# Kernel optimization log

Measured on AMD Instinct MI355X. Metric: run time of the kernel, lower is better.

Reference implementation:

```python
import jax, jax.numpy as jnp
import numpy as np

# ---- dims ----
V, VR, E, H, NF = 100000, 5000, 300, 256, 150
H2 = 2 * H  # 512


def _lstm_dir(x, Wih, Whh, b, h0, c0):
    # x: (T, B, E); returns hs (T, B, H), final (h, c)
    def step(carry, xt):
        h, c = carry
        z = xt @ Wih.T + h @ Whh.T + b
        i, f, g, o = jnp.split(z, 4, axis=-1)  # torch gate order i,f,g,o
        c = jax.nn.sigmoid(f) * c + jax.nn.sigmoid(i) * jnp.tanh(g)
        h = jax.nn.sigmoid(o) * jnp.tanh(c)
        return (h, c), h
    (hT, cT), hs = jax.lax.scan(step, (h0, c0), x)
    return hs, hT, cT


def bilstm(x, Wih_f, Whh_f, b_f, Wih_b, Whh_b, b_b, state=None):
    # x: (T, B, E) -> out (T, B, 2H), state tuple
    B = x.shape[1]
    if state is None:
        z = jnp.zeros((B, H), x.dtype)
        state = (z, z, z, z)
    h0f, c0f, h0b, c0b = state
    hs_f, hTf, cTf = _lstm_dir(x, Wih_f, Whh_f, b_f, h0f, c0f)
    hs_b, hTb, cTb = _lstm_dir(x[::-1], Wih_b, Whh_b, b_b, h0b, c0b)
    out = jnp.concatenate([hs_f, hs_b[::-1]], axis=-1)
    return out, (hTf, cTf, hTb, cTb)


def abwim_atten(question_out, word_rel, rela_rel, word_emb, rela_emb,
                Wih_f, Whh_f, b_f, Wih_b, Whh_b, b_b, W):
    # question_out: (B, 2H, Sq); word_rel (B,Sw), rela_rel (B,Sr) int
    rela = rela_emb[rela_rel.T]   # (Sr, B, E)
    word = word_emb[word_rel.T]   # (Sw, B, E)
    word_out, state = bilstm(word, Wih_f, Whh_f, b_f, Wih_b, Whh_b, b_b)
    rela_out, _ = bilstm(rela, Wih_f, Whh_f, b_f, Wih_b, Whh_b, b_b, state)
    relation = jnp.concatenate([rela_out, word_out], axis=0).transpose(1, 0, 2)  # (B, R, 2H)
    energy = jnp.einsum('brh,hk,bks->brs', relation, W, question_out)  # (B, R, Sq)
    B, R, Sq = energy.shape
    scale = 1.0 / np.sqrt(R).astype(np.float32)
    alpha = jax.nn.softmax(energy.reshape(B, R * Sq) * scale, axis=-1).reshape(B, R, Sq)
    # sum_r alpha[b,r,s] * relation[b,r,h] -> (B, 2H, Sq)
    return jnp.einsum('brs,brh->bhs', alpha, relation)


def setup_inputs():
    key = jax.random.key(0)
    ks = jax.random.split(key, 24)
    B, Sq, Sw, Sr = 64, 40, 12, 4
    s_emb, s_lstm, s_w = 0.05, 0.05, 0.04
    inp = {
        'question': jax.random.randint(ks[0], (B, Sq), 0, V),
        'word_relation': jax.random.randint(ks[1], (B, Sw), 0, V),
        'rela_relation': jax.random.randint(ks[2], (B, Sr), 0, VR),
        'word_previous': jax.random.randint(ks[3], (B, Sw), 0, V),
        'rela_previous': jax.random.randint(ks[4], (B, Sr), 0, VR),
        'word_emb': jax.random.normal(ks[5], (V, E), jnp.float32) * s_emb,
        'rela_emb': jax.random.normal(ks[6], (VR, E), jnp.float32) * s_emb,
        'Wih_f': jax.random.normal(ks[7], (4 * H, E), jnp.float32) * s_lstm,
        'Whh_f': jax.random.normal(ks[8], (4 * H, H), jnp.float32) * s_lstm,
        'b_f': jnp.zeros((4 * H,), jnp.float32),
        'Wih_b': jax.random.normal(ks[9], (4 * H, E), jnp.float32) * s_lstm,
        'Whh_b': jax.random.normal(ks[10], (4 * H, H), jnp.float32) * s_lstm,
        'b_b': jnp.zeros((4 * H,), jnp.float32),
        'W': jax.random.normal(ks[11], (H2, H2), jnp.float32) * s_w,
        'cnn1_w': jax.random.normal(ks[12], (NF, 2 * H2, 1), jnp.float32) * s_w,
        'cnn1_b': jnp.zeros((NF,), jnp.float32),
        'cnn2_w': jax.random.normal(ks[13], (NF, 2 * H2, 3), jnp.float32) * s_w,
        'cnn2_b': jnp.zeros((NF,), jnp.float32),
        'cnn3_w': jax.random.normal(ks[14], (NF, 2 * H2, 5), jnp.float32) * s_w,
        'cnn3_b': jnp.zeros((NF,), jnp.float32),
        'lin_w': jax.random.normal(ks[15], (1, NF), jnp.float32) * s_w,
        'lin2_w': jax.random.normal(ks[16], (H2, H2), jnp.float32) * s_w,
        'lin2_b': jnp.zeros((H2,), jnp.float32),
    }
    return inp


def _conv1d(x, w, b):
    # x: (B, C, L), w: (O, C, K)
    y = jax.lax.conv_general_dilated(x, w, (1,), 'VALID',
                                     dimension_numbers=('NCH', 'OIH', 'NCH'))
    return y + b[None, :, None]


def reference(question, word_relation, rela_relation, word_previous, rela_previous,
              word_emb, rela_emb, Wih_f, Whh_f, b_f, Wih_b, Whh_b, b_b, W,
              cnn1_w, cnn1_b, cnn2_w, cnn2_b, cnn3_w, cnn3_b, lin_w, lin2_w, lin2_b):
    lstm_p = (Wih_f, Whh_f, b_f, Wih_b, Whh_b, b_b)
    # question encoder (dropout is identity at eval)
    q = word_emb[question.T]                      # (Sq, B, E)
    q_out, _ = bilstm(q, *lstm_p)                 # (Sq, B, 2H)
    question_out = q_out.transpose(1, 2, 0)       # (B, 2H, Sq)
    # reduce one previous hop
    atten_prev = abwim_atten(question_out, word_previous, rela_previous,
                             word_emb, rela_emb, *lstm_p, W)
    qo = question_out - atten_prev
    qo = qo.transpose(0, 2, 1) @ lin2_w.T + lin2_b   # (B, Sq, 2H)
    question_out = qo.transpose(0, 2, 1)             # (B, 2H, Sq)
    # current relation attention
    atten_relation = abwim_atten(question_out, word_relation, rela_relation,
                                 word_emb, rela_emb, *lstm_p, W)
    M = jnp.concatenate([question_out, atten_relation], axis=1)  # (B, 4H, Sq)
    h1 = jnp.max(jax.nn.relu(_conv1d(M, cnn1_w, cnn1_b)), axis=2)  # (B, NF)
    h2 = jnp.max(jax.nn.relu(_conv1d(M, cnn2_w, cnn2_b)), axis=2)
    h3 = jnp.max(jax.nn.relu(_conv1d(M, cnn3_w, cnn3_b)), axis=2)
    h = jnp.maximum(jnp.maximum(h1, h2), h3)
    score = (h @ lin_w.T).squeeze(-1)  # (B,)
    return score
```

## Files before the change

### kernel.cpp

```cpp
#include <hip/hip_runtime.h>
#include <math.h>

#define NEG_INF (-3.402823466e+38f)

typedef __attribute__((ext_vector_type(8))) short short8;
typedef __attribute__((ext_vector_type(8))) unsigned short ushort8;
typedef __attribute__((ext_vector_type(4))) float f32x4;

constexpr int NTOK = 4608;
constexpr int BH = 64 * 256;

constexpr size_t OFF_WQ    = 0;
constexpr size_t OFF_B2    = OFF_WQ    + 524288;
constexpr size_t OFF_XB3T  = OFF_B2    + 2048;
constexpr size_t OFF_WB3T  = OFF_XB3T  + 983040;
constexpr size_t OFF_L2B3T = OFF_WB3T  + 393216;
constexpr size_t OFF_C1B3T = OFF_L2B3T + 393216;
constexpr size_t OFF_C2B3T = OFF_C1B3T + 294912;
constexpr size_t OFF_C3B3T = OFF_C2B3T + 884736;
constexpr size_t OFF_XHI   = OFF_C3B3T + 1474560;
constexpr size_t OFF_XLO   = OFF_XHI   + 737280;
constexpr size_t OFF_XP    = OFF_XLO   + 737280;
constexpr size_t OFF_HSQ   = OFF_XP    + 9437184;
constexpr size_t OFF_HSWP  = OFF_HSQ   + 1310720;
constexpr size_t OFF_HSRP  = OFF_HSWP  + 393216;
constexpr size_t OFF_HSWR  = OFF_HSRP  + 131072;
constexpr size_t OFF_HSRR  = OFF_HSWR  + 393216;
constexpr size_t OFF_CS    = OFF_HSRR  + 131072;
constexpr size_t OFF_RELP  = OFF_CS    + 163840;
constexpr size_t OFF_RELC  = OFF_RELP  + 524288;
constexpr size_t OFF_RELW  = OFF_RELC  + 524288;
constexpr size_t OFF_EN    = OFF_RELW  + 524288;

__device__ inline unsigned short f2bf(float f) {
  unsigned int u = __float_as_uint(f);
  u += 0x7FFFu + ((u >> 16) & 1u);
  return (unsigned short)(u >> 16);
}
__device__ inline float bf2f(unsigned short h) {
  return __uint_as_float(((unsigned int)h) << 16);
}
__device__ inline short8 mk8(unsigned long long a, unsigned long long b) {
  union { unsigned long long q[2]; short8 s; } u;
  u.q[0] = a; u.q[1] = b; return u.s;
}
#define ALD(p) __hip_atomic_load((p), __ATOMIC_RELAXED, __HIP_MEMORY_SCOPE_AGENT)

__global__ __launch_bounds__(256) void k_prep(
    const float* __restrict__ Whh_f, const float* __restrict__ Whh_b,
    const float* __restrict__ b_f,   const float* __restrict__ b_b,
    const float* __restrict__ Wih_f, const float* __restrict__ Wih_b,
    const float* __restrict__ Wat,   const float* __restrict__ l2w,
    const float* __restrict__ c1w, const float* __restrict__ c2w, const float* __restrict__ c3w,
    unsigned short* __restrict__ WHB, float* __restrict__ B2,
    unsigned short* __restrict__ XB3T, unsigned short* __restrict__ WB3T,
    unsigned short* __restrict__ L2B3T,
    unsigned short* __restrict__ C1B3T, unsigned short* __restrict__ C2B3T,
    unsigned short* __restrict__ C3B3T, int* __restrict__ bar) {
  if (blockIdx.x == 0 && threadIdx.x < 8)
    __hip_atomic_store(bar + threadIdx.x, 0, __ATOMIC_RELAXED, __HIP_MEMORY_SCOPE_AGENT);
  int idx = blockIdx.x * 256 + threadIdx.x;
  if (idx < 1048576) {
    int e = idx & 511;
    int k = e & 255, isLo = e >> 8;
    int row = (idx >> 9) & 63;
    int tile = (idx >> 15) & 15;
    int d = idx >> 19;
    int g = row >> 4, uu = row & 15;
    int u = tile * 16 + uu;
    const float* Wh = d ? Whh_b : Whh_f;
    float w = Wh[(size_t)(g * 256 + u) * 256 + k];
    unsigned short hi = f2bf(w);
    WHB[idx] = isLo ? f2bf(w - bf2f(hi)) : hi;
    return;
  }
  idx -= 1048576;
  if (idx < 2048) { B2[idx] = (idx < 1024) ? b_f[idx] : b_b[idx-1024]; return; }
  idx -= 2048;
  unsigned short* dst; int n, k, K;
  float w;
  if (idx < 655360) {
    n = idx / 320; k = idx % 320; K = 320; dst = XB3T;
    w = (k < 300) ? ((n < 1024) ? Wih_f[(size_t)n*300 + k] : Wih_b[(size_t)(n-1024)*300 + k]) : 0.f;
  } else if ((idx -= 655360) < 262144) {
    n = idx >> 9; k = idx & 511; K = 512; dst = WB3T;
    w = Wat[(size_t)k*512 + n];
  } else if ((idx -= 262144) < 262144) {
    n = idx >> 9; k = idx & 511; K = 512; dst = L2B3T;
    w = l2w[(size_t)n*512 + k];
  } else if ((idx -= 262144) < 196608) {
    n = idx >> 10; k = idx & 1023; K = 1024; dst = C1B3T;
    w = (n < 150) ? c1w[(size_t)n*1024 + k] : 0.f;
  } else if ((idx -= 196608) < 589824) {
    n = idx / 3072; k = idx % 3072; K = 3072; dst = C2B3T;
    int kw = k >> 10, c = k & 1023;
    w = (n < 150) ? c2w[((size_t)n*1024 + c)*3 + kw] : 0.f;
  } else if ((idx -= 589824) < 983040) {
    n = idx / 5120; k = idx % 5120; K = 5120; dst = C3B3T;
    int kw = k >> 10, c = k & 1023;
    w = (n < 150) ? c3w[((size_t)n*1024 + c)*5 + kw] : 0.f;
  } else return;
  unsigned short hi = f2bf(w);
  unsigned short lo = f2bf(w - bf2f(hi));
  size_t base = (size_t)n * (3*K);
  dst[base + k] = hi;
  dst[base + K + k] = lo;
  dst[base + 2*K + k] = hi;
}

__global__ __launch_bounds__(320) void k_gather(
    const int* __restrict__ q,  const int* __restrict__ wr, const int* __restrict__ rr,
    const int* __restrict__ wp, const int* __restrict__ rp,
    const float* __restrict__ we, const float* __restrict__ re,
    unsigned short* __restrict__ Xhi, unsigned short* __restrict__ Xlo) {
  int m = blockIdx.x, k = threadIdx.x;
  const float* emb; int row;
  if (m < 2560)      { int t=m>>6,    b=m&63; row = q [b*40+t]; emb = we; }
  else if (m < 3328) { int mm=m-2560; int t=mm>>6,b=mm&63; row = wp[b*12+t]; emb = we; }
  else if (m < 3584) { int mm=m-3328; int t=mm>>6,b=mm&63; row = rp[b*4 +t]; emb = re; }
  else if (m < 4352) { int mm=m-3584; int t=mm>>6,b=mm&63; row = wr[b*12+t]; emb = we; }
  else               { int mm=m-4352; int t=mm>>6,b=mm&63; row = rr[b*4 +t]; emb = re; }
  float v = (k < 300) ? emb[(size_t)row*300 + k] : 0.f;
  unsigned short hi = f2bf(v);
  Xhi[(size_t)m*320 + k] = hi;
  Xlo[(size_t)m*320 + k] = f2bf(v - bf2f(hi));
}

template<bool BIAS>
__global__ __launch_bounds__(256) void k_mgemm(
    const unsigned short* __restrict__ Ahi, const unsigned short* __restrict__ Alo, int lda,
    const unsigned short* __restrict__ Bt, const float* __restrict__ bias,
    float* __restrict__ C, int N, int K) {
  __shared__ unsigned short As[64 * 40];
  __shared__ unsigned short Bs[64 * 40];
  int tid = threadIdx.x;
  int wave = tid >> 6, lane = tid & 63;
  int quad = lane >> 4, l16 = lane & 15;
  int m0 = blockIdx.x << 6, n0 = blockIdx.y << 6;
  int K3 = 3 * K;
  int sr = tid >> 2;
  int sc = (tid & 3) << 3;
  f32x4 acc[4] = {};
  for (int k0 = 0; k0 < K3; k0 += 32) {
    int c = (k0 >= K) + (k0 >= 2*K);
    const unsigned short* Asrc = (c == 2) ? Alo : Ahi;
    int kk = k0 - c * K;
    ushort8 av = *(const ushort8*)(Asrc + (size_t)(m0 + sr) * lda + kk + sc);
    ushort8 bv = *(const ushort8*)(Bt + (size_t)(n0 + sr) * K3 + k0 + sc);
    *(ushort8*)&As[sr * 40 + sc] = av;
    *(ushort8*)&Bs[sr * 40 + sc] = bv;
    __syncthreads();
    short8 a  = *(const short8*)&As[(wave*16 + l16) * 40 + quad*8];
    short8 b0 = *(const short8*)&Bs[( 0 + l16) * 40 + quad*8];
    short8 b1 = *(const short8*)&Bs[(16 + l16) * 40 + quad*8];
    short8 b2 = *(const short8*)&Bs[(32 + l16) * 40 + quad*8];
    short8 b3 = *(const short8*)&Bs[(48 + l16) * 40 + quad*8];
    acc[0] = __builtin_amdgcn_mfma_f32_16x16x32_bf16(a, b0, acc[0], 0, 0, 0);
    acc[1] = __builtin_amdgcn_mfma_f32_16x16x32_bf16(a, b1, acc[1], 0, 0, 0);
    acc[2] = __builtin_amdgcn_mfma_f32_16x16x32_bf16(a, b2, acc[2], 0, 0, 0);
    acc[3] = __builtin_amdgcn_mfma_f32_16x16x32_bf16(a, b3, acc[3], 0, 0, 0);
    __syncthreads();
  }
  int row0 = m0 + wave * 16 + quad * 4;
#pragma unroll
  for (int t = 0; t < 4; t++) {
    int col = n0 + t * 16 + l16;
    float bb = BIAS ? bias[col] : 0.f;
#pragma unroll
    for (int r = 0; r < 4; r++)
      C[(size_t)(row0 + r) * N + col] = acc[t][r] + bb;
  }
}

__global__ __launch_bounds__(256) void k_cgemm(
    const unsigned short* __restrict__ Ahi, const unsigned short* __restrict__ Alo,
    const unsigned short* __restrict__ B1, const unsigned short* __restrict__ B2c,
    const unsigned short* __restrict__ B3,
    float* __restrict__ Y1, float* __restrict__ Y2, float* __restrict__ Y3) {
  __shared__ unsigned short As[64 * 40];
  __shared__ unsigned short Bs[64 * 40];
  int z = blockIdx.z;
  const unsigned short* Bt; float* Y; int K, sidx, chunk;
  if (z < 4)       { Bt = B1;  Y = Y1; K = 1024; sidx = z;      chunk = 768;  }
  else if (z < 12) { Bt = B2c; Y = Y2; K = 3072; sidx = z - 4;  chunk = 1152; }
  else             { Bt = B3;  Y = Y3; K = 5120; sidx = z - 12; chunk = 1920; }
  int K3 = 3 * K;
  int ks = sidx * chunk, ke = ks + chunk;
  int tid = threadIdx.x;
  int wave = tid >> 6, lane = tid & 63;
  int quad = lane >> 4, l16 = lane & 15;
  int m0 = blockIdx.x << 6, n0 = blockIdx.y << 6;
  int sr = tid >> 2;
  int sc = (tid & 3) << 3;
  f32x4 acc[4] = {};
  for (int k0 = ks; k0 < ke; k0 += 32) {
    int c = (k0 >= K) + (k0 >= 2*K);
    const unsigned short* Asrc = (c == 2) ? Alo : Ahi;
    int kk = k0 - c * K;
    ushort8 av = *(const ushort8*)(Asrc + (size_t)(m0 + sr) * 1024 + kk + sc);
    ushort8 bv = *(const ushort8*)(Bt + (size_t)(n0 + sr) * K3 + k0 + sc);
    *(ushort8*)&As[sr * 40 + sc] = av;
    *(ushort8*)&Bs[sr * 40 + sc] = bv;
    __syncthreads();
    short8 a  = *(const short8*)&As[(wave*16 + l16) * 40 + quad*8];
    short8 b0 = *(const short8*)&Bs[( 0 + l16) * 40 + quad*8];
    short8 b1 = *(const short8*)&Bs[(16 + l16) * 40 + quad*8];
    short8 b2 = *(const short8*)&Bs[(32 + l16) * 40 + quad*8];
    short8 b3 = *(const short8*)&Bs[(48 + l16) * 40 + quad*8];
    acc[0] = __builtin_amdgcn_mfma_f32_16x16x32_bf16(a, b0, acc[0], 0, 0, 0);
    acc[1] = __builtin_amdgcn_mfma_f32_16x16x32_bf16(a, b1, acc[1], 0, 0, 0);
    acc[2] = __builtin_amdgcn_mfma_f32_16x16x32_bf16(a, b2, acc[2], 0, 0, 0);
    acc[3] = __builtin_amdgcn_mfma_f32_16x16x32_bf16(a, b3, acc[3], 0, 0, 0);
    __syncthreads();
  }
  int row0 = m0 + wave * 16 + quad * 4;
#pragma unroll
  for (int t = 0; t < 4; t++) {
    int col = n0 + t * 16 + l16;
#pragma unroll
    for (int r = 0; r < 4; r++)
      atomicAdd(&Y[(size_t)(row0 + r) * 192 + col], acc[t][r]);
  }
}

__global__ __launch_bounds__(256) void k_zero(float* __restrict__ p, int n4) {
  int idx = blockIdx.x * 256 + threadIdx.x;
  if (idx < n4) *(float4*)(p + (size_t)idx * 4) = make_float4(0.f, 0.f, 0.f, 0.f);
}

__global__ __launch_bounds__(256, 1) void k_steps(
    const unsigned short* __restrict__ WHB, const float* __restrict__ XP,
    float* __restrict__ hsQ, float* __restrict__ hsWp, float* __restrict__ hsRp,
    float* __restrict__ hsWr, float* __restrict__ hsRr,
    unsigned short* __restrict__ Hhi, unsigned short* __restrict__ Hlo,
    int* __restrict__ bar) {
  int bid = blockIdx.x;
  int chain = bid & 7;
  if (chain >= 6) return;
  int tile = bid >> 3;
  int dir = chain & 1, fam = chain >> 1;
  int tid = threadIdx.x;
  int wave = tid >> 6, lane = tid & 63;
  int quad = lane >> 4, l16 = lane & 15;
  int u0 = tile << 4;

  const unsigned short* wsrc = WHB + (((size_t)dir * 16 + tile) << 15);
  short8 Bh[4][8], Bl[4][8];
#pragma unroll
  for (int nf = 0; nf < 4; nf++)
#pragma unroll
    for (int j = 0; j < 8; j++) {
      const unsigned short* wr = wsrc + (nf * 16 + l16) * 512 + j * 32 + quad * 8;
      Bh[nf][j] = *(const short8*)(wr);
      Bl[nf][j] = *(const short8*)(wr + 256);
    }

  int nsteps = (fam == 0) ? 40 : 16;
  float creg[4] = {0.f, 0.f, 0.f, 0.f};
  int row64 = (wave * 16 + l16) * 64 + quad * 2;

  for (int cs = 0; cs < nsteps; cs++) {
    int t, T, seg; float* hsb;
    if (fam == 0)     { t = cs;      T = 40; seg = 0;                         hsb = hsQ + (size_t)dir * 40 * BH; }
    else if (cs < 12) { t = cs;      T = 12; seg = (fam == 1) ? 2560 : 3584;  hsb = ((fam == 1) ? hsWp : hsWr) + (size_t)dir * 12 * BH; }
    else              { t = cs - 12; T = 4;  seg = (fam == 1) ? 3328 : 4352;  hsb = ((fam == 1) ? hsRp : hsRr) + (size_t)dir * 4 * BH; }
    int t_in = dir ? (T - 1 - t) : t;
    int u = u0 + l16;
    const float* xb = XP + (size_t)(seg + t_in * 64) * 2048 + dir * 1024 + u;
    float xi[4], xf[4], xg[4], xo[4];
#pragma unroll
    for (int r = 0; r < 4; r++) {
      const float* xr = xb + (size_t)(wave * 16 + quad * 4 + r) * 2048;
      xi[r] = xr[0]; xf[r] = xr[256]; xg[r] = xr[512]; xo[r] = xr[768];
    }

    f32x4 acc[4] = {};
    if (cs > 0) {
      if (tid == 0) {
        int tgt = 16 * cs;
        while (__hip_atomic_load(bar + chain, __ATOMIC_RELAXED, __HIP_MEMORY_SCOPE_AGENT) < tgt)
          __builtin_amdgcn_s_sleep(1);
      }
      __syncthreads();
      size_t slotq = (size_t)(chain * 2 + ((cs - 1) & 1)) * 4096;
      const unsigned long long* ph = (const unsigned long long*)Hhi + slotq + row64;
      const unsigned long long* pl = (const unsigned long long*)Hlo + slotq + row64;
      unsigned long long rv[32];
#pragma unroll
      for (int j = 0; j < 8; j++) { rv[2*j] = ALD(ph + 8*j); rv[2*j+1] = ALD(ph + 8*j + 1); }
#pragma unroll
      for (int j = 0; j < 8; j++) { rv[16+2*j] = ALD(pl + 8*j); rv[16+2*j+1] = ALD(pl + 8*j + 1); }
      short8 ah[8], al[8];
#pragma unroll
      for (int j = 0; j < 8; j++) { ah[j] = mk8(rv[2*j], rv[2*j+1]); al[j] = mk8(rv[16+2*j], rv[16+2*j+1]); }
#pragma unroll
      for (int j = 0; j < 8; j++) {
        acc[0] = __builtin_amdgcn_mfma_f32_16x16x32_bf16(ah[j], Bh[0][j], acc[0], 0, 0, 0);
        acc[1] = __builtin_amdgcn_mfma_f32_16x16x32_bf16(ah[j], Bh[1][j], acc[1], 0, 0, 0);
        acc[2] = __builtin_amdgcn_mfma_f32_16x16x32_bf16(ah[j], Bh[2][j], acc[2], 0, 0, 0);
        acc[3] = __builtin_amdgcn_mfma_f32_16x16x32_bf16(ah[j], Bh[3][j], acc[3], 0, 0, 0);
      }
#pragma unroll
      for (int j = 0; j < 8; j++) {
        acc[0] = __builtin_amdgcn_mfma_f32_16x16x32_bf16(ah[j], Bl[0][j], acc[0], 0, 0, 0);
        acc[1] = __builtin_amdgcn_mfma_f32_16x16x32_bf16(ah[j], Bl[1][j], acc[1], 0, 0, 0);
        acc[2] = __builtin_amdgcn_mfma_f32_16x16x32_bf16(ah[j], Bl[2][j], acc[2], 0, 0, 0);
        acc[3] = __builtin_amdgcn_mfma_f32_16x16x32_bf16(ah[j], Bl[3][j], acc[3], 0, 0, 0);
      }
#pragma unroll
      for (int j = 0; j < 8; j++) {
        acc[0] = __builtin_amdgcn_mfma_f32_16x16x32_bf16(al[j], Bh[0][j], acc[0], 0, 0, 0);
        acc[1] = __builtin_amdgcn_mfma_f32_16x16x32_bf16(al[j], Bh[1][j], acc[1], 0, 0, 0);
        acc[2] = __builtin_amdgcn_mfma_f32_16x16x32_bf16(al[j], Bh[2][j], acc[2], 0, 0, 0);
        acc[3] = __builtin_amdgcn_mfma_f32_16x16x32_bf16(al[j], Bh[3][j], acc[3], 0, 0, 0);
      }
    }
    float* hout = hsb + (size_t)t * BH + u;
    size_t oslot = (size_t)(chain * 2 + (cs & 1)) << 14;
    unsigned short* oh = Hhi + oslot;
    unsigned short* ol = Hlo + oslot;
#pragma unroll
    for (int r = 0; r < 4; r++) {
      int b = wave * 16 + quad * 4 + r;
      float zi = acc[0][r] + xi[r];
      float zf = acc[1][r] + xf[r];
      float zg = acc[2][r] + xg[r];
      float zo = acc[3][r] + xo[r];
      float gi = 1.f / (1.f + expf(-zi));
      float gf = 1.f / (1.f + expf(-zf));
      float go = 1.f / (1.f + expf(-zo));
      float gg = tanhf(zg);
      float cn = gf * creg[r] + gi * gg;
      float hn = go * tanhf(cn);
      creg[r] = cn;
      unsigned short h16 = f2bf(hn);
      unsigned short l16v = f2bf(hn - bf2f(h16));
      unsigned int pk = (unsigned int)h16 | ((unsigned int)l16v << 16);
      unsigned int pw = (unsigned int)__shfl_xor((int)pk, 1, 64);
      if ((lane & 1) == 0) {
        unsigned int hw = (pk & 0xFFFFu) | (pw << 16);
        unsigned int lw = (pk >> 16) | (pw & 0xFFFF0000u);
        __hip_atomic_store((unsigned int*)(oh + b * 256 + u), hw,
                           __ATOMIC_RELAXED, __HIP_MEMORY_SCOPE_AGENT);
        __hip_atomic_store((unsigned int*)(ol + b * 256 + u), lw,
                           __ATOMIC_RELAXED, __HIP_MEMORY_SCOPE_AGENT);
      }
      hout[(size_t)b * 256] = hn;
    }
    if (cs + 1 < nsteps) {
      __syncthreads();
      if (tid == 0)
        __hip_atomic_fetch_add(bar + chain, 1, __ATOMIC_RELAXED, __HIP_MEMORY_SCOPE_AGENT);
    }
  }
}

__global__ __launch_bounds__(256) void k_qo1(const float* __restrict__ hsQ, float* __restrict__ QT) {
  int idx = blockIdx.x * 256 + threadIdx.x;
  if (idx >= 64*40*512) return;
  int h = idx & 511; int t2 = idx >> 9; int s = t2 % 40; int b = t2 / 40;
  float v;
  if (h < 256) v = hsQ[(size_t)s * BH + b*256 + h];
  else         v = hsQ[(size_t)40 * BH + (size_t)(39 - s) * BH + b*256 + (h - 256)];
  QT[idx] = v;
}

__global__ __launch_bounds__(256) void k_rel(
    const float* __restrict__ hsWp, const float* __restrict__ hsRp,
    const float* __restrict__ hsWr, const float* __restrict__ hsRr,
    float* __restrict__ RELP, float* __restrict__ RELC,
    unsigned short* __restrict__ RPhi, unsigned short* __restrict__ RPlo,
    unsigned short* __restrict__ RChi, unsigned short* __restrict__ RClo) {
  int idx0 = blockIdx.x * 256 + threadIdx.x;
  if (idx0 >= 2*64*16*512) return;
  int call = idx0 >= 64*16*512;
  int idx = idx0 - call * 64*16*512;
  int h = idx & 511; int t2 = idx >> 9; int r = t2 & 15; int b = t2 >> 4;
  const float* hsW = call ? hsWr : hsWp;
  const float* hsR = call ? hsRr : hsRp;
  float v;
  if (r < 4) {
    if (h < 256) v = hsR[(size_t)r * BH + b*256 + h];
    else         v = hsR[(size_t)4 * BH + (size_t)(3 - r) * BH + b*256 + (h - 256)];
  } else {
    int t = r - 4;
    if (h < 256) v = hsW[(size_t)t * BH + b*256 + h];
    else         v = hsW[(size_t)12 * BH + (size_t)(11 - t) * BH + b*256 + (h - 256)];
  }
  unsigned short hi = f2bf(v);
  unsigned short lo = f2bf(v - bf2f(hi));
  if (call) { RELC[idx] = v; RChi[idx] = hi; RClo[idx] = lo; }
  else      { RELP[idx] = v; RPhi[idx] = hi; RPlo[idx] = lo; }
}

__global__ __launch_bounds__(256) void k_energy(
    const float* __restrict__ relW, const float* __restrict__ QT, float* __restrict__ EN) {
  int idx = blockIdx.x * 256 + threadIdx.x;
  if (idx >= 64*16*40) return;
  int s = idx % 40; int t = idx / 40; int r = t & 15; int b = t >> 4;
  const float* rw = relW + (size_t)(b*16 + r) * 512;
  const float* qv = QT   + (size_t)(b*40 + s) * 512;
  float acc = 0.f;
#pragma unroll 4
  for (int k = 0; k < 512; k += 4) {
    float4 a = *(const float4*)(rw + k);
    float4 c = *(const float4*)(qv + k);
    acc += a.x*c.x + a.y*c.y + a.z*c.z + a.w*c.w;
  }
  EN[idx] = acc;
}

__global__ __launch_bounds__(256) void k_softmax(float* __restrict__ EN) {
  int b = blockIdx.x; int tid = threadIdx.x;
  float* e = EN + b * 640;
  float v0 = e[tid] * 0.25f, v1 = e[tid + 256] * 0.25f;
  float v2 = (tid < 128) ? e[tid + 512] * 0.25f : NEG_INF;
  __shared__ float sh[256];
  sh[tid] = fmaxf(v0, fmaxf(v1, v2));
  __syncthreads();
  for (int st = 128; st > 0; st >>= 1) { if (tid < st) sh[tid] = fmaxf(sh[tid], sh[tid+st]); __syncthreads(); }
  float m = sh[0];
  __syncthreads();
  float e0 = expf(v0 - m), e1 = expf(v1 - m);
  float e2 = (tid < 128) ? expf(v2 - m) : 0.f;
  sh[tid] = e0 + e1 + e2;
  __syncthreads();
  for (int st = 128; st > 0; st >>= 1) { if (tid < st) sh[tid] += sh[tid+st]; __syncthreads(); }
  float inv = 1.f / sh[0];
  e[tid] = e0 * inv; e[tid + 256] = e1 * inv;
  if (tid < 128) e[tid + 512] = e2 * inv;
}

__global__ __launch_bounds__(256) void k_atten(
    const float* __restrict__ AL, const float* __restrict__ REL, float* __restrict__ ATT) {
  int idx = blockIdx.x * 256 + threadIdx.x;
  if (idx >= 64*40*512) return;
  int h = idx & 511; int t2 = idx >> 9; int s = t2 % 40; int b = t2 / 40;
  const float* al = AL + b * 640 + s;
  const float* rl = REL + (size_t)b * 16 * 512 + h;
  float acc = 0.f;
#pragma unroll
  for (int r = 0; r < 16; r++) acc += al[r*40] * rl[r*512];
  ATT[idx] = acc;
}

__global__ __launch_bounds__(256) void k_sub(
    const float* __restrict__ QT, const float* __restrict__ ATT,
    unsigned short* __restrict__ Dhi, unsigned short* __restrict__ Dlo) {
  int idx = blockIdx.x * 256 + threadIdx.x;
  if (idx >= 64*40*512) return;
  float v = QT[idx] - ATT[idx];
  unsigned short hi = f2bf(v);
  Dhi[idx] = hi; Dlo[idx] = f2bf(v - bf2f(hi));
}

__global__ __launch_bounds__(256) void k_m2(
    const float* __restrict__ QO2, const float* __restrict__ ATT,
    unsigned short* __restrict__ M2hi, unsigned short* __restrict__ M2lo) {
  int idx = blockIdx.x * 256 + threadIdx.x;
  if (idx >= 2626048) return;
  float v = 0.f;
  if (idx < 2621440) {
    int c = idx & 1023; int m = idx >> 10;
    v = (c < 512) ? QO2[(size_t)m*512 + c] : ATT[(size_t)m*512 + (c - 512)];
  }
  unsigned short hi = f2bf(v);
  M2hi[idx] = hi; M2lo[idx] = f2bf(v - bf2f(hi));
}

__global__ __launch_bounds__(256) void k_pool(
    const float* __restrict__ Y1, const float* __restrict__ Y2, const float* __restrict__ Y3,
    const float* __restrict__ b1, const float* __restrict__ b2, const float* __restrict__ b3,
    const float* __restrict__ lw, float* __restrict__ out) {
  int b = blockIdx.x, o = threadIdx.x;
  float hv = 0.f;
  if (o < 150) {
    const float* y1 = Y1 + (size_t)b*40*192 + o;
    const float* y2 = Y2 + (size_t)b*40*192 + o;
    const float* y3 = Y3 + (size_t)b*40*192 + o;
    float m1 = NEG_INF, m2 = NEG_INF, m3 = NEG_INF;
#pragma unroll 4
    for (int l = 0; l < 40; l++) m1 = fmaxf(m1, y1[l*192]);
#pragma unroll 2
    for (int l = 0; l < 38; l++) m2 = fmaxf(m2, y2[l*192]);
#pragma unroll 2
    for (int l = 0; l < 36; l++) m3 = fmaxf(m3, y3[l*192]);
    float h = fmaxf(fmaxf(m1 + b1[o], m2 + b2[o]), m3 + b3[o]);
    hv = fmaxf(h, 0.f) * lw[o];
  }
  __shared__ float sh[256];
  sh[threadIdx.x] = hv;
  __syncthreads();
  for (int st = 128; st > 0; st >>= 1) { if (threadIdx.x < st) sh[threadIdx.x] += sh[threadIdx.x+st]; __syncthreads(); }
  if (threadIdx.x == 0) out[b] = sh[0];
}

extern "C" void kernel_launch(void* const* d_in, const int* in_sizes, int n_in,
                              void* d_out, int out_size, void* d_ws, size_t ws_size,
                              hipStream_t stream) {
  const int*   q    = (const int*)d_in[0];
  const int*   wrel = (const int*)d_in[1];
  const int*   rrel = (const int*)d_in[2];
  const int*   wprv = (const int*)d_in[3];
  const int*   rprv = (const int*)d_in[4];
  const float* we   = (const float*)d_in[5];
  const float* re   = (const float*)d_in[6];
  const float* Wih_f= (const float*)d_in[7];
  const float* Whh_f= (const float*)d_in[8];
  const float* b_f  = (const float*)d_in[9];
  const float* Wih_b= (const float*)d_in[10];
  const float* Whh_b= (const float*)d_in[11];
  const float* b_b  = (const float*)d_in[12];
  const float* W    = (const float*)d_in[13];
  const float* c1w  = (const float*)d_in[14];
  const float* c1b  = (const float*)d_in[15];
  const float* c2w  = (const float*)d_in[16];
  const float* c2b  = (const float*)d_in[17];
  const float* c3w  = (const float*)d_in[18];
  const float* c3b  = (const float*)d_in[19];
  const float* lw   = (const float*)d_in[20];
  const float* l2w  = (const float*)d_in[21];
  const float* l2b  = (const float*)d_in[22];
  float* out = (float*)d_out;
  float* ws  = (float*)d_ws;

  unsigned short* WHB = (unsigned short*)(ws + OFF_WQ);
  float* B2   = ws + OFF_B2;
  unsigned short* XB3T  = (unsigned short*)(ws + OFF_XB3T);
  unsigned short* WB3T  = (unsigned short*)(ws + OFF_WB3T);
  unsigned short* L2B3T = (unsigned short*)(ws + OFF_L2B3T);
  unsigned short* C1B3T = (unsigned short*)(ws + OFF_C1B3T);
  unsigned short* C2B3T = (unsigned short*)(ws + OFF_C2B3T);
  unsigned short* C3B3T = (unsigned short*)(ws + OFF_C3B3T);
  unsigned short* Xhi   = (unsigned short*)(ws + OFF_XHI);
  unsigned short* Xlo   = (unsigned short*)(ws + OFF_XLO);
  float* XP   = ws + OFF_XP;
  float* HSQ  = ws + OFF_HSQ;
  float* HSWP = ws + OFF_HSWP;
  float* HSRP = ws + OFF_HSRP;
  float* HSWR = ws + OFF_HSWR;
  float* HSRR = ws + OFF_HSRR;
  int*   bar  = (int*)(ws + OFF_CS);
  float* RELP = ws + OFF_RELP;
  float* RELC = ws + OFF_RELC;
  float* RELW = ws + OFF_RELW;
  float* EN   = ws + OFF_EN;
  unsigned short* Hhi = (unsigned short*)(ws + OFF_RELP);
  unsigned short* Hlo = Hhi + 196608;
  float* QO1  = XP;
  float* ATT  = XP + 1310720;
  float* QO2  = XP + 2621440;
  unsigned short* Dhi  = (unsigned short*)(XP + 3932160);
  unsigned short* Dlo  = (unsigned short*)(XP + 4587520);
  unsigned short* RPhi = (unsigned short*)(XP + 5242880);
  unsigned short* RPlo = (unsigned short*)(XP + 5505024);
  unsigned short* RChi = (unsigned short*)(XP + 5767168);
  unsigned short* RClo = (unsigned short*)(XP + 6029312);
  unsigned short* M2hi = (unsigned short*)(XP + 5242880);
  unsigned short* M2lo = (unsigned short*)(XP + 6555904);
  float* Y1   = XP + 7868928;
  float* Y2   = XP + 8360448;
  float* Y3   = XP + 8851968;

  k_prep<<<15624, 256, 0, stream>>>(Whh_f, Whh_b, b_f, b_b, Wih_f, Wih_b, W, l2w,
                                    c1w, c2w, c3w,
                                    WHB, B2, XB3T, WB3T, L2B3T, C1B3T, C2B3T, C3B3T, bar);
  k_gather<<<NTOK, 320, 0, stream>>>(q, wrel, rrel, wprv, rprv, we, re, Xhi, Xlo);
  { dim3 g(72, 32); k_mgemm<true><<<g, 256, 0, stream>>>(Xhi, Xlo, 320, XB3T, B2, XP, 2048, 320); }

  k_steps<<<128, 256, 0, stream>>>(WHB, XP, HSQ, HSWP, HSRP, HSWR, HSRR, Hhi, Hlo, bar);

  k_qo1<<<5120, 256, 0, stream>>>(HSQ, QO1);
  k_rel<<<4096, 256, 0, stream>>>(HSWP, HSRP, HSWR, HSRR, RELP, RELC, RPhi, RPlo, RChi, RClo);

  { dim3 g(16, 8); k_mgemm<false><<<g, 256, 0, stream>>>(RPhi, RPlo, 512, WB3T, nullptr, RELW, 512, 512); }
  k_energy<<<160, 256, 0, stream>>>(RELW, QO1, EN);
  k_softmax<<<64, 256, 0, stream>>>(EN);
  k_atten<<<5120, 256, 0, stream>>>(EN, RELP, ATT);
  k_sub<<<5120, 256, 0, stream>>>(QO1, ATT, Dhi, Dlo);
  { dim3 g(40, 8); k_mgemm<true><<<g, 256, 0, stream>>>(Dhi, Dlo, 512, L2B3T, l2b, QO2, 512, 512); }

  { dim3 g(16, 8); k_mgemm<false><<<g, 256, 0, stream>>>(RChi, RClo, 512, WB3T, nullptr, RELW, 512, 512); }
  k_energy<<<160, 256, 0, stream>>>(RELW, QO2, EN);
  k_softmax<<<64, 256, 0, stream>>>(EN);
  k_atten<<<5120, 256, 0, stream>>>(EN, RELC, ATT);

  k_m2<<<10258, 256, 0, stream>>>(QO2, ATT, M2hi, M2lo);
  k_zero<<<1440, 256, 0, stream>>>(Y1, 368640);
  { dim3 g(40, 3, 20); k_cgemm<<<g, 256, 0, stream>>>(M2hi, M2lo, C1B3T, C2B3T, C3B3T, Y1, Y2, Y3); }
  k_pool<<<64, 256, 0, stream>>>(Y1, Y2, Y3, c1b, c2b, c3b, lw, out);
}
```

Measured before the change: 789.8 us.

## Replace per-chain atomic counter barrier with per-tile padded flags in LSTM steps

The recurrent-step kernel previously synchronized the 16 tile blocks of each chain through one shared atomic counter that every block incremented and polled. Each block now stores its step number into its own cache-line-padded flag, with double-buffered slots. Sixteen threads each poll one producer's flag, which removes contention on a single atomic. The h-state exchange stores are also moved ahead of the hs output writes so the next step's data is published earlier. The change adds more flag traffic and more polling threads per block.

```diff
diff --git a/kernel.cpp b/kernel.cpp
--- a/kernel.cpp
+++ b/kernel.cpp
@@ -56,10 +56,10 @@
     unsigned short* __restrict__ XB3T, unsigned short* __restrict__ WB3T,
     unsigned short* __restrict__ L2B3T,
     unsigned short* __restrict__ C1B3T, unsigned short* __restrict__ C2B3T,
-    unsigned short* __restrict__ C3B3T, int* __restrict__ bar) {
-  if (blockIdx.x == 0 && threadIdx.x < 8)
-    __hip_atomic_store(bar + threadIdx.x, 0, __ATOMIC_RELAXED, __HIP_MEMORY_SCOPE_AGENT);
+    unsigned short* __restrict__ C3B3T, int* __restrict__ flags) {
   int idx = blockIdx.x * 256 + threadIdx.x;
+  if (idx < 3072)
+    __hip_atomic_store(flags + idx * 16, 0, __ATOMIC_RELAXED, __HIP_MEMORY_SCOPE_AGENT);
   if (idx < 1048576) {
     int e = idx & 511;
     int k = e & 255, isLo = e >> 8;
@@ -233,7 +233,7 @@
     float* __restrict__ hsQ, float* __restrict__ hsWp, float* __restrict__ hsRp,
     float* __restrict__ hsWr, float* __restrict__ hsRr,
     unsigned short* __restrict__ Hhi, unsigned short* __restrict__ Hlo,
-    int* __restrict__ bar) {
+    int* __restrict__ flags) {
   int bid = blockIdx.x;
   int chain = bid & 7;
   if (chain >= 6) return;
@@ -276,10 +276,10 @@
 
     f32x4 acc[4] = {};
     if (cs > 0) {
-      if (tid == 0) {
-        int tgt = 16 * cs;
-        while (__hip_atomic_load(bar + chain, __ATOMIC_RELAXED, __HIP_MEMORY_SCOPE_AGENT) < tgt)
-          __builtin_amdgcn_s_sleep(1);
+      if (tid < 16) {
+        const int* fp = flags + ((((chain << 1) | ((cs - 1) & 1)) * 16 + tid) << 4);
+        while (__hip_atomic_load(fp, __ATOMIC_RELAXED, __HIP_MEMORY_SCOPE_AGENT) < cs)
+          __builtin_amdgcn_s_sleep(2);
       }
       __syncthreads();
       size_t slotq = (size_t)(chain * 2 + ((cs - 1) & 1)) * 4096;
@@ -315,13 +315,9 @@
         acc[3] = __builtin_amdgcn_mfma_f32_16x16x32_bf16(al[j], Bh[3][j], acc[3], 0, 0, 0);
       }
     }
-    float* hout = hsb + (size_t)t * BH + u;
-    size_t oslot = (size_t)(chain * 2 + (cs & 1)) << 14;
-    unsigned short* oh = Hhi + oslot;
-    unsigned short* ol = Hlo + oslot;
+    float hnv[4];
 #pragma unroll
     for (int r = 0; r < 4; r++) {
-      int b = wave * 16 + quad * 4 + r;
       float zi = acc[0][r] + xi[r];
       float zf = acc[1][r] + xf[r];
       float zg = acc[2][r] + xg[r];
@@ -331,10 +327,17 @@
       float go = 1.f / (1.f + expf(-zo));
       float gg = tanhf(zg);
       float cn = gf * creg[r] + gi * gg;
-      float hn = go * tanhf(cn);
+      hnv[r] = go * tanhf(cn);
       creg[r] = cn;
-      unsigned short h16 = f2bf(hn);
-      unsigned short l16v = f2bf(hn - bf2f(h16));
+    }
+    size_t oslot = (size_t)(chain * 2 + (cs & 1)) << 14;
+    unsigned short* oh = Hhi + oslot;
+    unsigned short* ol = Hlo + oslot;
+#pragma unroll
+    for (int r = 0; r < 4; r++) {
+      int b = wave * 16 + quad * 4 + r;
+      unsigned short h16 = f2bf(hnv[r]);
+      unsigned short l16v = f2bf(hnv[r] - bf2f(h16));
       unsigned int pk = (unsigned int)h16 | ((unsigned int)l16v << 16);
       unsigned int pw = (unsigned int)__shfl_xor((int)pk, 1, 64);
       if ((lane & 1) == 0) {
@@ -345,12 +348,18 @@
         __hip_atomic_store((unsigned int*)(ol + b * 256 + u), lw,
                            __ATOMIC_RELAXED, __HIP_MEMORY_SCOPE_AGENT);
       }
-      hout[(size_t)b * 256] = hn;
+    }
+    float* hout = hsb + (size_t)t * BH + u;
+#pragma unroll
+    for (int r = 0; r < 4; r++) {
+      int b = wave * 16 + quad * 4 + r;
+      hout[(size_t)b * 256] = hnv[r];
     }
     if (cs + 1 < nsteps) {
       __syncthreads();
       if (tid == 0)
-        __hip_atomic_fetch_add(bar + chain, 1, __ATOMIC_RELAXED, __HIP_MEMORY_SCOPE_AGENT);
+        __hip_atomic_store(flags + ((((chain << 1) | (cs & 1)) * 16 + tile) << 4), cs + 1,
+                           __ATOMIC_RELAXED, __HIP_MEMORY_SCOPE_AGENT);
     }
   }
 }
@@ -540,7 +549,7 @@
   float* HSRP = ws + OFF_HSRP;
   float* HSWR = ws + OFF_HSWR;
   float* HSRR = ws + OFF_HSRR;
-  int*   bar  = (int*)(ws + OFF_CS);
+  int*   flags = (int*)(ws + OFF_CS);
   float* RELP = ws + OFF_RELP;
   float* RELC = ws + OFF_RELC;
   float* RELW = ws + OFF_RELW;
@@ -564,11 +573,11 @@
 
   k_prep<<<15624, 256, 0, stream>>>(Whh_f, Whh_b, b_f, b_b, Wih_f, Wih_b, W, l2w,
                                     c1w, c2w, c3w,
-                                    WHB, B2, XB3T, WB3T, L2B3T, C1B3T, C2B3T, C3B3T, bar);
+                                    WHB, B2, XB3T, WB3T, L2B3T, C1B3T, C2B3T, C3B3T, flags);
   k_gather<<<NTOK, 320, 0, stream>>>(q, wrel, rrel, wprv, rprv, we, re, Xhi, Xlo);
   { dim3 g(72, 32); k_mgemm<true><<<g, 256, 0, stream>>>(Xhi, Xlo, 320, XB3T, B2, XP, 2048, 320); }
 
-  k_steps<<<128, 256, 0, stream>>>(WHB, XP, HSQ, HSWP, HSRP, HSWR, HSRR, Hhi, Hlo, bar);
+  k_steps<<<128, 256, 0, stream>>>(WHB, XP, HSQ, HSWP, HSRP, HSWR, HSRR, Hhi, Hlo, flags);
 
   k_qo1<<<5120, 256, 0, stream>>>(HSQ, QO1);
   k_rel<<<4096, 256, 0, stream>>>(HSWP, HSRP, HSWR, HSRR, RELP, RELC, RPhi, RPlo, RChi, RClo);
```

New measurement: 785.1 us. About the same (-0.6%).
